# Kernel tuning notes

Hardware: AMD Instinct MI355X
Metric: run time of the kernel (lower is better)

Reference implementation:

```python
import jax, jax.numpy as jnp
import numpy as np

N = 50000          # nodes
E = 800000         # edges (avg degree 16)
T = 4              # edge types (edge_attr_dim)
H = 8              # heads
C1 = 16            # state_dim (per-head channels, layer 1)
C2 = 8             # out_dim  (per-head channels, layer 2)
D = 128            # node_attr_dim
NEG = -1e9         # masked-attention logit
LRELU_SLOPE = 0.2  # PyG GATConv default negative_slope


def setup_inputs() -> dict:
    key = jax.random.key(0)
    ks = jax.random.split(key, 12)
    x = jax.random.normal(ks[0], (N, D), jnp.float32)
    edge_src = jax.random.randint(ks[1], (E,), 0, N, jnp.int32)
    edge_dst = jax.random.randint(ks[2], (E,), 0, N, jnp.int32)
    edge_type = jax.random.randint(ks[3], (E,), 0, T, jnp.int32)
    W1 = jax.random.normal(ks[4], (T, D, H * C1), jnp.float32) * (1.0 / np.sqrt(D))
    a1_src = jax.random.normal(ks[5], (T, H, C1), jnp.float32) * 0.1
    a1_dst = jax.random.normal(ks[6], (T, H, C1), jnp.float32) * 0.1
    b1 = jnp.zeros((T, H * C1), jnp.float32)
    W2 = jax.random.normal(ks[7], (T, H * C1, H * C2), jnp.float32) * (1.0 / np.sqrt(H * C1))
    a2_src = jax.random.normal(ks[8], (T, H, C2), jnp.float32) * 0.1
    a2_dst = jax.random.normal(ks[9], (T, H, C2), jnp.float32) * 0.1
    b2 = jnp.zeros((T, H * C2), jnp.float32)
    return dict(x=x, edge_src=edge_src, edge_dst=edge_dst, edge_type=edge_type,
                W1=W1, a1_src=a1_src, a1_dst=a1_dst, b1=b1,
                W2=W2, a2_src=a2_src, a2_dst=a2_dst, b2=b2)


def gat_conv(x_in, W, a_src, a_dst, b, src, dst, mask, n):
    """One PyG-style GATConv (concat heads, eval mode) on masked edge list."""
    heads, c = a_src.shape
    h = (x_in @ W).reshape(n, heads, c)                       # [N,H,C]
    s_src = jnp.sum(h * a_src, axis=-1)                        # [N,H]
    s_dst = jnp.sum(h * a_dst, axis=-1)                        # [N,H]
    e = jax.nn.leaky_relu(s_src[src] + s_dst[dst], LRELU_SLOPE)  # [Et,H]
    e = jnp.where(mask[:, None], e, NEG)
    m = jax.ops.segment_max(e, dst, num_segments=n)            # [N,H]
    p = jnp.exp(e - m[dst]) * mask[:, None].astype(e.dtype)    # unnorm softmax
    denom = jax.ops.segment_sum(p, dst, num_segments=n)        # [N,H]
    msg = p[:, :, None] * h[src]                               # [Et,H,C]
    agg = jax.ops.segment_sum(msg, dst, num_segments=n)        # [N,H,C]
    out = agg / denom[:, :, None]
    return out.reshape(n, heads * c) + b


def reference(x, edge_src, edge_dst, edge_type, W1, a1_src, a1_dst, b1,
              W2, a2_src, a2_dst, b2):
    n = x.shape[0]
    loops = jnp.arange(n, dtype=edge_src.dtype)
    src = jnp.concatenate([edge_src, loops])   # self-loops appended (PyG default)
    dst = jnp.concatenate([edge_dst, loops])
    ones = jnp.ones((n,), bool)
    outs = []
    for t in range(T):
        mask = jnp.concatenate([edge_type == t, ones])
        h1 = gat_conv(x, W1[t], a1_src[t], a1_dst[t], b1[t], src, dst, mask, n)
        h1 = jax.nn.relu(h1)
        h2 = gat_conv(h1, W2[t], a2_src[t], a2_dst[t], b2[t], src, dst, mask, n)
        outs.append(h2)
    return jnp.concatenate(outs, axis=1)       # [N, T*H*C2]
```

## Files before the change

kernel.cpp:

```cpp
#include <hip/hip_runtime.h>
#include <cstddef>

constexpr int NN  = 50000;
constexpr int NE  = 800000;
constexpr int NT  = 4;
constexpr int NH  = 8;
constexpr int C1  = 16;
constexpr int C2  = 8;
constexpr int DD  = 128;
constexpr int HC1 = NH * C1;
constexpr int HC2 = NH * C2;
constexpr int NB  = NT * NN;
constexpr int CAP = 28;
constexpr float SLOPE = 0.2f;

constexpr int G_SCA1 = 1563;
constexpr int G_SCA2 = 1562;
constexpr int E_SPLIT = G_SCA1 * 256;
constexpr int G_CONV = NN * DD / 4 / 256;
constexpr int G_P1   = NT * 16384 / 256;
constexpr int G_P2   = NT * 8192 / 256;
constexpr int G_PREP = G_SCA1 + G_CONV + G_P1 + G_P2;
constexpr int G_GEMM = (NN + 63) / 64;
constexpr int G_GAT1 = NN / 16;
constexpr int G_GAT2 = (NN + 31) / 32;

using short8 = __attribute__((ext_vector_type(8))) short;
using f32x4  = __attribute__((ext_vector_type(4))) float;

__device__ __forceinline__ float lrelu(float x) { return x > 0.f ? x : SLOPE * x; }
__device__ __forceinline__ float bfl(unsigned u) { return __uint_as_float(u << 16); }
__device__ __forceinline__ float bfh(unsigned u) { return __uint_as_float(u & 0xffff0000u); }
__device__ __forceinline__ unsigned short f2bf(float f) {
    unsigned u = __float_as_uint(f);
    return (unsigned short)((u + 0x7fffu + ((u >> 16) & 1u)) >> 16);
}

__device__ __forceinline__ void scatter_edge(int i, const int* __restrict__ esrc,
        const int* __restrict__ edst, const int* __restrict__ etyp,
        unsigned* __restrict__ bkt) {
    int bk = etyp[i] * NN + edst[i];
    unsigned* bp = bkt + (size_t)bk * 16;
    int slot = atomicAdd(reinterpret_cast<int*>(bp), 1);
    if (slot < CAP)
        reinterpret_cast<unsigned short*>(bp)[2 + slot] = (unsigned short)esrc[i];
}

__global__ __launch_bounds__(256) void prep_kernel(const float* __restrict__ x,
        unsigned short* __restrict__ xb, const float* __restrict__ W1,
        unsigned short* __restrict__ wp1, const float* __restrict__ W2,
        unsigned short* __restrict__ wp2, const int* __restrict__ esrc,
        const int* __restrict__ edst, const int* __restrict__ etyp,
        unsigned* __restrict__ bkt) {
    const int b = blockIdx.x, tid = threadIdx.x;
    if (b < G_SCA1) {
        scatter_edge(b * 256 + tid, esrc, edst, etyp, bkt);
    } else if (b < G_SCA1 + G_CONV) {
        int i = (b - G_SCA1) * 256 + tid;
        float4 v = reinterpret_cast<const float4*>(x)[i];
        uint2 o;
        o.x = (unsigned)f2bf(v.x) | ((unsigned)f2bf(v.y) << 16);
        o.y = (unsigned)f2bf(v.z) | ((unsigned)f2bf(v.w) << 16);
        reinterpret_cast<uint2*>(xb)[i] = o;
    } else if (b < G_SCA1 + G_CONV + G_P1) {
        int i = (b - G_SCA1 - G_CONV) * 256 + tid;
        int t = i >> 14, r = i & 16383;
        int ntl = r >> 11, ks = (r >> 9) & 3, lane = (r >> 3) & 63, j = r & 7;
        int col = ntl * 16 + (lane & 15);
        int k   = ks * 32 + (lane >> 4) * 8 + j;
        wp1[i] = f2bf(W1[((size_t)t * DD + k) * HC1 + col]);
    } else {
        int i = (b - G_SCA1 - G_CONV - G_P1) * 256 + tid;
        int t = i >> 13, r = i & 8191;
        int ntl = r >> 11, ks = (r >> 9) & 3, lane = (r >> 3) & 63, j = r & 7;
        int col = ntl * 16 + (lane & 15);
        int k   = ks * 32 + (lane >> 4) * 8 + j;
        wp2[i] = f2bf(W2[((size_t)t * HC1 + k) * HC2 + col]);
    }
}

__device__ __forceinline__ void gemm1_body(int bx, int tid,
        const unsigned short* __restrict__ A, const unsigned short* __restrict__ Wp,
        const float* __restrict__ as, const float* __restrict__ ad,
        unsigned short* __restrict__ outb, float* __restrict__ ss,
        float* __restrict__ sd) {
    constexpr int J = HC1, CPH = C1, NTILE = J / 16;
    const int wave = tid >> 6;
    const int lane = tid & 63;
    const int q    = lane >> 4;
    const int c    = lane & 15;
    const int rowbase = bx * 64 + wave * 16;

    int arow = rowbase + c; if (arow >= NN) arow = NN - 1;
    const unsigned short* ap = A + (size_t)arow * DD + q * 8;
    short8 afrag[4];
    #pragma unroll
    for (int ks = 0; ks < 4; ++ks)
        afrag[ks] = *reinterpret_cast<const short8*>(ap + ks * 32);

    f32x4 acc[NTILE];
    #pragma unroll
    for (int ntl = 0; ntl < NTILE; ++ntl) acc[ntl] = (f32x4){0.f, 0.f, 0.f, 0.f};

    const short8* wp = reinterpret_cast<const short8*>(Wp) + lane;
    #pragma unroll
    for (int ntl = 0; ntl < NTILE; ++ntl)
        #pragma unroll
        for (int ks = 0; ks < 4; ++ks) {
            short8 b = wp[(ntl * 4 + ks) * 64];
            acc[ntl] = __builtin_amdgcn_mfma_f32_16x16x32_bf16(afrag[ks], b, acc[ntl], 0, 0, 0);
        }

    #pragma unroll
    for (int ntl = 0; ntl < NTILE; ++ntl) {
        int head = ntl;
        float av = as[head * CPH + c];
        float dv = ad[head * CPH + c];
        float t0[4], t1[4];
        #pragma unroll
        for (int reg = 0; reg < 4; ++reg) {
            int row = rowbase + q * 4 + reg;
            if (row < NN) outb[(size_t)row * J + ntl * 16 + c] = f2bf(acc[ntl][reg]);
            t0[reg] = acc[ntl][reg] * av;
            t1[reg] = acc[ntl][reg] * dv;
        }
        #pragma unroll
        for (int m = 1; m < CPH; m <<= 1)
            #pragma unroll
            for (int reg = 0; reg < 4; ++reg) {
                t0[reg] += __shfl_xor(t0[reg], m);
                t1[reg] += __shfl_xor(t1[reg], m);
            }
        if (c == 0) {
            #pragma unroll
            for (int reg = 0; reg < 4; ++reg) {
                int row = rowbase + q * 4 + reg;
                if (row < NN) { ss[row * NH + head] = t0[reg]; sd[row * NH + head] = t1[reg]; }
            }
        }
    }
}

__global__ __launch_bounds__(256) void scatgemm_kernel(
        const int* __restrict__ esrc, const int* __restrict__ edst,
        const int* __restrict__ etyp, unsigned* __restrict__ bkt,
        const unsigned short* __restrict__ xb, const unsigned short* __restrict__ wp1t,
        const float* __restrict__ as, const float* __restrict__ ad,
        unsigned short* __restrict__ h1, float* __restrict__ ss,
        float* __restrict__ sd) {
    const int b = blockIdx.x, tid = threadIdx.x;
    if (b < G_SCA2) {
        scatter_edge(E_SPLIT + b * 256 + tid, esrc, edst, etyp, bkt);
    } else {
        gemm1_body(b - G_SCA2, tid, xb, wp1t, as, ad, h1, ss, sd);
    }
}

template<int TPN>
__device__ __forceinline__ void gather_body(const unsigned* __restrict__ bkt, int bk,
        int q, int head, const float* __restrict__ ss, float sdn,
        const uint4* __restrict__ h4, float& den, float acc[8]) {
    const uint4* lp = reinterpret_cast<const uint4*>(bkt) + (size_t)bk * 4;
    uint4 w0 = lp[0], w1 = lp[1], w2 = lp[2], w3 = lp[3];
    int deg = (int)w0.x; if (deg > CAP) deg = CAP;
    unsigned ws[14] = {w0.y, w0.z, w0.w, w1.x, w1.y, w1.z, w1.w,
                       w2.x, w2.y, w2.z, w2.w, w3.x, w3.y, w3.z};
    #pragma unroll
    for (int c = 0; c < 7; ++c) {
        if (c * 4 >= deg) break;
        unsigned lo = ws[c * 2], hi = ws[c * 2 + 1];
        int sv[4] = {(int)(lo & 0xffff), (int)(lo >> 16),
                     (int)(hi & 0xffff), (int)(hi >> 16)};
        #pragma unroll
        for (int j = 0; j < 4; ++j) {
            if (c * 4 + j < deg) {
                int s = sv[j];
                float pp = __expf(lrelu(ss[s * NH + head] + sdn));
                uint4 hv = h4[(size_t)s * TPN + q];
                den += pp;
                acc[0] += pp * bfl(hv.x); acc[1] += pp * bfh(hv.x);
                acc[2] += pp * bfl(hv.y); acc[3] += pp * bfh(hv.y);
                acc[4] += pp * bfl(hv.z); acc[5] += pp * bfh(hv.z);
                acc[6] += pp * bfl(hv.w); acc[7] += pp * bfh(hv.w);
            }
        }
    }
}

__global__ __launch_bounds__(256) void g1g2_kernel(
        const unsigned* __restrict__ bkt, int t,
        const float* __restrict__ ss1, const float* __restrict__ sd1,
        const unsigned short* __restrict__ h1, const float* __restrict__ b1t,
        const unsigned short* __restrict__ wp2t,
        const float* __restrict__ as2, const float* __restrict__ ad2,
        unsigned short* __restrict__ h2, float* __restrict__ ss2,
        float* __restrict__ sd2) {
    __shared__ unsigned short lt[16][136];
    const int tid   = threadIdx.x;
    const int node0 = blockIdx.x * 16;
    const int nl    = tid >> 4;
    const int node  = node0 + nl;
    const int q     = tid & 15;
    const int head  = q >> 1;
    const int bk    = t * NN + node;
    const float sdn = sd1[node * NH + head];
    const uint4* __restrict__ h4 = reinterpret_cast<const uint4*>(h1);

    float p = __expf(lrelu(ss1[node * NH + head] + sdn));
    float den = p;
    uint4 hv = h4[(size_t)node * 16 + q];
    float acc[8];
    acc[0] = p * bfl(hv.x); acc[1] = p * bfh(hv.x);
    acc[2] = p * bfl(hv.y); acc[3] = p * bfh(hv.y);
    acc[4] = p * bfl(hv.z); acc[5] = p * bfh(hv.z);
    acc[6] = p * bfl(hv.w); acc[7] = p * bfh(hv.w);
    gather_body<16>(bkt, bk, q, head, ss1, sdn, h4, den, acc);

    float inv = 1.f / den;
    uint4 ov;
    {
        float o[8];
        #pragma unroll
        for (int i = 0; i < 8; ++i)
            o[i] = fmaxf(acc[i] * inv + b1t[q * 8 + i], 0.f);
        ov.x = (unsigned)f2bf(o[0]) | ((unsigned)f2bf(o[1]) << 16);
        ov.y = (unsigned)f2bf(o[2]) | ((unsigned)f2bf(o[3]) << 16);
        ov.z = (unsigned)f2bf(o[4]) | ((unsigned)f2bf(o[5]) << 16);
        ov.w = (unsigned)f2bf(o[6]) | ((unsigned)f2bf(o[7]) << 16);
    }
    *reinterpret_cast<uint4*>(&lt[nl][q * 8]) = ov;
    __syncthreads();

    const int wave = tid >> 6;
    const int lane = tid & 63;
    const int quad = lane >> 4;
    const int c    = lane & 15;
    short8 af[4];
    #pragma unroll
    for (int ks = 0; ks < 4; ++ks)
        af[ks] = *reinterpret_cast<const short8*>(&lt[c][ks * 32 + quad * 8]);
    f32x4 cacc = (f32x4){0.f, 0.f, 0.f, 0.f};
    const short8* wp = reinterpret_cast<const short8*>(wp2t) + lane;
    #pragma unroll
    for (int ks = 0; ks < 4; ++ks)
        cacc = __builtin_amdgcn_mfma_f32_16x16x32_bf16(af[ks], wp[(wave * 4 + ks) * 64], cacc, 0, 0, 0);

    const int col   = wave * 16 + c;
    const int head2 = col >> 3;
    const int cm    = c & 7;
    float av = as2[head2 * C2 + cm];
    float dv = ad2[head2 * C2 + cm];
    float t0[4], t1[4];
    #pragma unroll
    for (int reg = 0; reg < 4; ++reg) {
        int row = node0 + quad * 4 + reg;
        h2[(size_t)row * HC2 + col] = f2bf(cacc[reg]);
        t0[reg] = cacc[reg] * av;
        t1[reg] = cacc[reg] * dv;
    }
    #pragma unroll
    for (int m = 1; m < C2; m <<= 1)
        #pragma unroll
        for (int reg = 0; reg < 4; ++reg) {
            t0[reg] += __shfl_xor(t0[reg], m);
            t1[reg] += __shfl_xor(t1[reg], m);
        }
    if (cm == 0) {
        #pragma unroll
        for (int reg = 0; reg < 4; ++reg) {
            int row = node0 + quad * 4 + reg;
            ss2[row * NH + head2] = t0[reg];
            sd2[row * NH + head2] = t1[reg];
        }
    }
}

__global__ __launch_bounds__(256) void gat2gemm_kernel(
        const unsigned* __restrict__ bkt, int t,
        const float* __restrict__ ss2, const float* __restrict__ sd2,
        const unsigned short* __restrict__ h2, const float* __restrict__ b2t,
        float* __restrict__ out,
        const unsigned short* __restrict__ xb, const unsigned short* __restrict__ wp1n,
        const float* __restrict__ asn, const float* __restrict__ adn,
        unsigned short* __restrict__ h1, float* __restrict__ ss1,
        float* __restrict__ sd1) {
    const int b = blockIdx.x, tid = threadIdx.x;
    if (b >= G_GAT2) {
        gemm1_body(b - G_GAT2, tid, xb, wp1n, asn, adn, h1, ss1, sd1);
        return;
    }
    const int node = b * 32 + (tid >> 3);
    if (node >= NN) return;
    const int q    = tid & 7;
    const int head = q;
    const int bk   = t * NN + node;
    const float sdn = sd2[node * NH + head];
    const uint4* __restrict__ h4 = reinterpret_cast<const uint4*>(h2);

    float p = __expf(lrelu(ss2[node * NH + head] + sdn));
    float den = p;
    uint4 hv = h4[(size_t)node * 8 + q];
    float acc[8];
    acc[0] = p * bfl(hv.x); acc[1] = p * bfh(hv.x);
    acc[2] = p * bfl(hv.y); acc[3] = p * bfh(hv.y);
    acc[4] = p * bfl(hv.z); acc[5] = p * bfh(hv.z);
    acc[6] = p * bfl(hv.w); acc[7] = p * bfh(hv.w);
    gather_body<8>(bkt, bk, q, head, ss2, sdn, h4, den, acc);

    float inv = 1.f / den;
    float o[8];
    #pragma unroll
    for (int i = 0; i < 8; ++i) o[i] = acc[i] * inv + b2t[q * 8 + i];
    float* op = out + (size_t)node * (NT * HC2) + t * HC2 + q * 8;
    reinterpret_cast<float4*>(op)[0] = make_float4(o[0], o[1], o[2], o[3]);
    reinterpret_cast<float4*>(op)[1] = make_float4(o[4], o[5], o[6], o[7]);
}

extern "C" void kernel_launch(void* const* d_in, const int* in_sizes, int n_in,
                              void* d_out, int out_size, void* d_ws, size_t ws_size,
                              hipStream_t stream) {
    const float* x    = (const float*)d_in[0];
    const int*   esrc = (const int*)d_in[1];
    const int*   edst = (const int*)d_in[2];
    const int*   etyp = (const int*)d_in[3];
    const float* W1   = (const float*)d_in[4];
    const float* a1s  = (const float*)d_in[5];
    const float* a1d  = (const float*)d_in[6];
    const float* b1   = (const float*)d_in[7];
    const float* W2   = (const float*)d_in[8];
    const float* a2s  = (const float*)d_in[9];
    const float* a2d  = (const float*)d_in[10];
    const float* b2   = (const float*)d_in[11];
    float* out = (float*)d_out;

    char* base = (char*)d_ws;
    unsigned short* xb  = (unsigned short*)(base);
    unsigned short* h1b = (unsigned short*)(base + 12800000);
    unsigned short* h2b = (unsigned short*)(base + 25600000);
    float* ss1 = (float*)(base + 32000000);
    float* sd1 = (float*)(base + 33600000);
    float* ss2 = (float*)(base + 35200000);
    float* sd2 = (float*)(base + 36800000);
    unsigned* bkt = (unsigned*)(base + 38400000);
    unsigned short* wp1 = (unsigned short*)(base + 51200000);
    unsigned short* wp2 = (unsigned short*)(base + 51331072);

    dim3 blk(256);

    hipMemsetAsync(bkt, 0, (size_t)NB * 64, stream);
    hipLaunchKernelGGL(prep_kernel, dim3(G_PREP), blk, 0, stream,
                       x, xb, W1, wp1, W2, wp2, esrc, edst, etyp, bkt);
    hipLaunchKernelGGL(scatgemm_kernel, dim3(G_SCA2 + G_GEMM), blk, 0, stream,
                       esrc, edst, etyp, bkt,
                       xb, wp1, a1s, a1d, h1b, ss1, sd1);

    for (int t = 0; t < NT; ++t) {
        hipLaunchKernelGGL(g1g2_kernel, dim3(G_GAT1), blk, 0, stream,
                           bkt, t, ss1, sd1, h1b, b1 + t * HC1,
                           wp2 + (size_t)t * 8192,
                           a2s + t * NH * C2, a2d + t * NH * C2,
                           h2b, ss2, sd2);
        int tn = t + 1;
        int grid = G_GAT2 + (tn < NT ? G_GEMM : 0);
        hipLaunchKernelGGL(gat2gemm_kernel, dim3(grid), blk, 0, stream,
                           bkt, t, ss2, sd2, h2b, b2 + t * HC2, out,
                           xb, wp1 + (size_t)(tn < NT ? tn : 0) * 16384,
                           a1s + (tn < NT ? tn : 0) * NH * C1,
                           a1d + (tn < NT ? tn : 0) * NH * C1,
                           h1b, ss1, sd1);
    }
}
```

Baseline: 345.5 us.

## Pipeline GAT stages across edge types with double buffers and packed half scores

The per-type launch sequence becomes a five-step software pipeline. Each mega-kernel runs layer-1 gather+GEMM2 for type t, layer-2 gather for type t-1, and GEMM1 for type t+1, with h1/h2/score buffers double-buffered. The separate x-to-bf16 conversion pass is removed and the conversion happens inside GEMM1 loads. Attention scores are packed as half2 (src,dst), and buckets shrink to a 56-byte stride with capacity 26. The scatter handles four edges per thread. The main risks are lost precision in the half-stored scores and dropped edges at high degree from the smaller capacity.

```diff
diff --git a/kernel.cpp b/kernel.cpp
--- a/kernel.cpp
+++ b/kernel.cpp
@@ -1,4 +1,5 @@
 #include <hip/hip_runtime.h>
+#include <hip/hip_fp16.h>
 #include <cstddef>
 
 constexpr int NN  = 50000;
@@ -10,67 +11,68 @@
 constexpr int DD  = 128;
 constexpr int HC1 = NH * C1;
 constexpr int HC2 = NH * C2;
-constexpr int NB  = NT * NN;
-constexpr int CAP = 28;
+constexpr int CAP = 26;
+constexpr int BSTRIDE = 56;
 constexpr float SLOPE = 0.2f;
 
-constexpr int G_SCA1 = 1563;
-constexpr int G_SCA2 = 1562;
-constexpr int E_SPLIT = G_SCA1 * 256;
-constexpr int G_CONV = NN * DD / 4 / 256;
+constexpr int G_SCA  = 391;
+constexpr int E_SPLIT = G_SCA * 1024;
 constexpr int G_P1   = NT * 16384 / 256;
 constexpr int G_P2   = NT * 8192 / 256;
-constexpr int G_PREP = G_SCA1 + G_CONV + G_P1 + G_P2;
 constexpr int G_GEMM = (NN + 63) / 64;
 constexpr int G_GAT1 = NN / 16;
 constexpr int G_GAT2 = (NN + 31) / 32;
 
 using short8 = __attribute__((ext_vector_type(8))) short;
 using f32x4  = __attribute__((ext_vector_type(4))) float;
+typedef unsigned short u16;
 
 __device__ __forceinline__ float lrelu(float x) { return x > 0.f ? x : SLOPE * x; }
 __device__ __forceinline__ float bfl(unsigned u) { return __uint_as_float(u << 16); }
 __device__ __forceinline__ float bfh(unsigned u) { return __uint_as_float(u & 0xffff0000u); }
-__device__ __forceinline__ unsigned short f2bf(float f) {
+__device__ __forceinline__ u16 f2bf(float f) {
     unsigned u = __float_as_uint(f);
-    return (unsigned short)((u + 0x7fffu + ((u >> 16) & 1u)) >> 16);
-}
-
-__device__ __forceinline__ void scatter_edge(int i, const int* __restrict__ esrc,
+    return (u16)((u + 0x7fffu + ((u >> 16) & 1u)) >> 16);
+}
+
+__device__ __forceinline__ void scatter4(int e0, int elim, const int* __restrict__ esrc,
         const int* __restrict__ edst, const int* __restrict__ etyp,
         unsigned* __restrict__ bkt) {
-    int bk = etyp[i] * NN + edst[i];
-    unsigned* bp = bkt + (size_t)bk * 16;
-    int slot = atomicAdd(reinterpret_cast<int*>(bp), 1);
-    if (slot < CAP)
-        reinterpret_cast<unsigned short*>(bp)[2 + slot] = (unsigned short)esrc[i];
-}
-
-__global__ __launch_bounds__(256) void prep_kernel(const float* __restrict__ x,
-        unsigned short* __restrict__ xb, const float* __restrict__ W1,
-        unsigned short* __restrict__ wp1, const float* __restrict__ W2,
-        unsigned short* __restrict__ wp2, const int* __restrict__ esrc,
-        const int* __restrict__ edst, const int* __restrict__ etyp,
-        unsigned* __restrict__ bkt) {
+    int bk[4], src[4];
+    bool v[4];
+    #pragma unroll
+    for (int k = 0; k < 4; ++k) {
+        int i = e0 + k * 256;
+        v[k] = i < elim;
+        bk[k] = 0; src[k] = 0;
+        if (v[k]) { bk[k] = etyp[i] * NN + edst[i]; src[k] = esrc[i]; }
+    }
+    int slot[4];
+    #pragma unroll
+    for (int k = 0; k < 4; ++k)
+        if (v[k]) slot[k] = atomicAdd((int*)((char*)bkt + (size_t)bk[k] * BSTRIDE), 1);
+    #pragma unroll
+    for (int k = 0; k < 4; ++k)
+        if (v[k] && slot[k] < CAP)
+            ((u16*)((char*)bkt + (size_t)bk[k] * BSTRIDE))[2 + slot[k]] = (u16)src[k];
+}
+
+__global__ __launch_bounds__(256) void prep_kernel(const float* __restrict__ W1,
+        u16* __restrict__ wp1, const float* __restrict__ W2, u16* __restrict__ wp2,
+        const int* __restrict__ esrc, const int* __restrict__ edst,
+        const int* __restrict__ etyp, unsigned* __restrict__ bkt) {
     const int b = blockIdx.x, tid = threadIdx.x;
-    if (b < G_SCA1) {
-        scatter_edge(b * 256 + tid, esrc, edst, etyp, bkt);
-    } else if (b < G_SCA1 + G_CONV) {
-        int i = (b - G_SCA1) * 256 + tid;
-        float4 v = reinterpret_cast<const float4*>(x)[i];
-        uint2 o;
-        o.x = (unsigned)f2bf(v.x) | ((unsigned)f2bf(v.y) << 16);
-        o.y = (unsigned)f2bf(v.z) | ((unsigned)f2bf(v.w) << 16);
-        reinterpret_cast<uint2*>(xb)[i] = o;
-    } else if (b < G_SCA1 + G_CONV + G_P1) {
-        int i = (b - G_SCA1 - G_CONV) * 256 + tid;
+    if (b < G_SCA) {
+        scatter4(b * 1024 + tid, E_SPLIT, esrc, edst, etyp, bkt);
+    } else if (b < G_SCA + G_P1) {
+        int i = (b - G_SCA) * 256 + tid;
         int t = i >> 14, r = i & 16383;
         int ntl = r >> 11, ks = (r >> 9) & 3, lane = (r >> 3) & 63, j = r & 7;
         int col = ntl * 16 + (lane & 15);
         int k   = ks * 32 + (lane >> 4) * 8 + j;
         wp1[i] = f2bf(W1[((size_t)t * DD + k) * HC1 + col]);
     } else {
-        int i = (b - G_SCA1 - G_CONV - G_P1) * 256 + tid;
+        int i = (b - G_SCA - G_P1) * 256 + tid;
         int t = i >> 13, r = i & 8191;
         int ntl = r >> 11, ks = (r >> 9) & 3, lane = (r >> 3) & 63, j = r & 7;
         int col = ntl * 16 + (lane & 15);
@@ -79,12 +81,10 @@
     }
 }
 
-__device__ __forceinline__ void gemm1_body(int bx, int tid,
-        const unsigned short* __restrict__ A, const unsigned short* __restrict__ Wp,
-        const float* __restrict__ as, const float* __restrict__ ad,
-        unsigned short* __restrict__ outb, float* __restrict__ ss,
-        float* __restrict__ sd) {
-    constexpr int J = HC1, CPH = C1, NTILE = J / 16;
+__device__ __forceinline__ void gemm1_body(int bx, int tid, const float* __restrict__ x,
+        const u16* __restrict__ Wp, const float* __restrict__ as,
+        const float* __restrict__ ad, u16* __restrict__ h1w, __half2* __restrict__ s1w) {
+    constexpr int NTILE = HC1 / 16;
     const int wave = tid >> 6;
     const int lane = tid & 63;
     const int q    = lane >> 4;
@@ -92,16 +92,23 @@
     const int rowbase = bx * 64 + wave * 16;
 
     int arow = rowbase + c; if (arow >= NN) arow = NN - 1;
-    const unsigned short* ap = A + (size_t)arow * DD + q * 8;
+    const float* xp = x + (size_t)arow * DD + q * 8;
     short8 afrag[4];
     #pragma unroll
-    for (int ks = 0; ks < 4; ++ks)
-        afrag[ks] = *reinterpret_cast<const short8*>(ap + ks * 32);
+    for (int ks = 0; ks < 4; ++ks) {
+        float4 f0 = *reinterpret_cast<const float4*>(xp + ks * 32);
+        float4 f1 = *reinterpret_cast<const float4*>(xp + ks * 32 + 4);
+        short8 a;
+        a[0] = (short)f2bf(f0.x); a[1] = (short)f2bf(f0.y);
+        a[2] = (short)f2bf(f0.z); a[3] = (short)f2bf(f0.w);
+        a[4] = (short)f2bf(f1.x); a[5] = (short)f2bf(f1.y);
+        a[6] = (short)f2bf(f1.z); a[7] = (short)f2bf(f1.w);
+        afrag[ks] = a;
+    }
 
     f32x4 acc[NTILE];
     #pragma unroll
     for (int ntl = 0; ntl < NTILE; ++ntl) acc[ntl] = (f32x4){0.f, 0.f, 0.f, 0.f};
-
     const short8* wp = reinterpret_cast<const short8*>(Wp) + lane;
     #pragma unroll
     for (int ntl = 0; ntl < NTILE; ++ntl)
@@ -114,18 +121,18 @@
     #pragma unroll
     for (int ntl = 0; ntl < NTILE; ++ntl) {
         int head = ntl;
-        float av = as[head * CPH + c];
-        float dv = ad[head * CPH + c];
+        float av = as[head * C1 + c];
+        float dv = ad[head * C1 + c];
         float t0[4], t1[4];
         #pragma unroll
         for (int reg = 0; reg < 4; ++reg) {
             int row = rowbase + q * 4 + reg;
-            if (row < NN) outb[(size_t)row * J + ntl * 16 + c] = f2bf(acc[ntl][reg]);
+            if (row < NN) h1w[(size_t)row * HC1 + ntl * 16 + c] = f2bf(acc[ntl][reg]);
             t0[reg] = acc[ntl][reg] * av;
             t1[reg] = acc[ntl][reg] * dv;
         }
         #pragma unroll
-        for (int m = 1; m < CPH; m <<= 1)
+        for (int m = 1; m < C1; m <<= 1)
             #pragma unroll
             for (int reg = 0; reg < 4; ++reg) {
                 t0[reg] += __shfl_xor(t0[reg], m);
@@ -135,7 +142,9 @@
             #pragma unroll
             for (int reg = 0; reg < 4; ++reg) {
                 int row = rowbase + q * 4 + reg;
-                if (row < NN) { ss[row * NH + head] = t0[reg]; sd[row * NH + head] = t1[reg]; }
+                if (row < NN)
+                    s1w[row * NH + head] =
+                        __halves2half2(__float2half_rn(t0[reg]), __float2half_rn(t1[reg]));
             }
         }
     }
@@ -144,39 +153,39 @@
 __global__ __launch_bounds__(256) void scatgemm_kernel(
         const int* __restrict__ esrc, const int* __restrict__ edst,
         const int* __restrict__ etyp, unsigned* __restrict__ bkt,
-        const unsigned short* __restrict__ xb, const unsigned short* __restrict__ wp1t,
+        const float* __restrict__ x, const u16* __restrict__ wp1t,
         const float* __restrict__ as, const float* __restrict__ ad,
-        unsigned short* __restrict__ h1, float* __restrict__ ss,
-        float* __restrict__ sd) {
+        u16* __restrict__ h1, __half2* __restrict__ ss) {
     const int b = blockIdx.x, tid = threadIdx.x;
-    if (b < G_SCA2) {
-        scatter_edge(E_SPLIT + b * 256 + tid, esrc, edst, etyp, bkt);
+    if (b < G_SCA) {
+        scatter4(E_SPLIT + b * 1024 + tid, NE, esrc, edst, etyp, bkt);
     } else {
-        gemm1_body(b - G_SCA2, tid, xb, wp1t, as, ad, h1, ss, sd);
+        gemm1_body(b - G_SCA, tid, x, wp1t, as, ad, h1, ss);
     }
 }
 
 template<int TPN>
 __device__ __forceinline__ void gather_body(const unsigned* __restrict__ bkt, int bk,
-        int q, int head, const float* __restrict__ ss, float sdn,
+        int q, int head, const __half2* __restrict__ s, float sdn,
         const uint4* __restrict__ h4, float& den, float acc[8]) {
-    const uint4* lp = reinterpret_cast<const uint4*>(bkt) + (size_t)bk * 4;
-    uint4 w0 = lp[0], w1 = lp[1], w2 = lp[2], w3 = lp[3];
-    int deg = (int)w0.x; if (deg > CAP) deg = CAP;
-    unsigned ws[14] = {w0.y, w0.z, w0.w, w1.x, w1.y, w1.z, w1.w,
-                       w2.x, w2.y, w2.z, w2.w, w3.x, w3.y, w3.z};
+    const uint2* bp = reinterpret_cast<const uint2*>((const char*)bkt + (size_t)bk * BSTRIDE);
+    unsigned w[14];
+    #pragma unroll
+    for (int i = 0; i < 7; ++i) { uint2 u = bp[i]; w[2 * i] = u.x; w[2 * i + 1] = u.y; }
+    int deg = (int)w[0]; if (deg > CAP) deg = CAP;
     #pragma unroll
     for (int c = 0; c < 7; ++c) {
         if (c * 4 >= deg) break;
-        unsigned lo = ws[c * 2], hi = ws[c * 2 + 1];
+        unsigned lo = w[1 + 2 * c];
+        unsigned hi = (c < 6) ? w[2 + 2 * c] : 0u;
         int sv[4] = {(int)(lo & 0xffff), (int)(lo >> 16),
                      (int)(hi & 0xffff), (int)(hi >> 16)};
         #pragma unroll
         for (int j = 0; j < 4; ++j) {
             if (c * 4 + j < deg) {
-                int s = sv[j];
-                float pp = __expf(lrelu(ss[s * NH + head] + sdn));
-                uint4 hv = h4[(size_t)s * TPN + q];
+                int sn = sv[j];
+                float pp = __expf(lrelu(__low2float(s[sn * NH + head]) + sdn));
+                uint4 hv = h4[(size_t)sn * TPN + q];
                 den += pp;
                 acc[0] += pp * bfl(hv.x); acc[1] += pp * bfh(hv.x);
                 acc[2] += pp * bfl(hv.y); acc[3] += pp * bfh(hv.y);
@@ -187,26 +196,23 @@
     }
 }
 
-__global__ __launch_bounds__(256) void g1g2_kernel(
-        const unsigned* __restrict__ bkt, int t,
-        const float* __restrict__ ss1, const float* __restrict__ sd1,
-        const unsigned short* __restrict__ h1, const float* __restrict__ b1t,
-        const unsigned short* __restrict__ wp2t,
+__device__ __forceinline__ void g1g2_body(int bx, int tid, const unsigned* __restrict__ bkt,
+        int t, const __half2* __restrict__ s1r, const u16* __restrict__ h1r,
+        const float* __restrict__ b1t, const u16* __restrict__ wp2t,
         const float* __restrict__ as2, const float* __restrict__ ad2,
-        unsigned short* __restrict__ h2, float* __restrict__ ss2,
-        float* __restrict__ sd2) {
-    __shared__ unsigned short lt[16][136];
-    const int tid   = threadIdx.x;
-    const int node0 = blockIdx.x * 16;
+        u16* __restrict__ h2w, __half2* __restrict__ s2w) {
+    __shared__ u16 lt[16][136];
+    const int node0 = bx * 16;
     const int nl    = tid >> 4;
     const int node  = node0 + nl;
     const int q     = tid & 15;
     const int head  = q >> 1;
     const int bk    = t * NN + node;
-    const float sdn = sd1[node * NH + head];
-    const uint4* __restrict__ h4 = reinterpret_cast<const uint4*>(h1);
-
-    float p = __expf(lrelu(ss1[node * NH + head] + sdn));
+    const __half2 sown = s1r[node * NH + head];
+    const float sdn = __high2float(sown);
+    const uint4* __restrict__ h4 = reinterpret_cast<const uint4*>(h1r);
+
+    float p = __expf(lrelu(__low2float(sown) + sdn));
     float den = p;
     uint4 hv = h4[(size_t)node * 16 + q];
     float acc[8];
@@ -214,7 +220,7 @@
     acc[2] = p * bfl(hv.y); acc[3] = p * bfh(hv.y);
     acc[4] = p * bfl(hv.z); acc[5] = p * bfh(hv.z);
     acc[6] = p * bfl(hv.w); acc[7] = p * bfh(hv.w);
-    gather_body<16>(bkt, bk, q, head, ss1, sdn, h4, den, acc);
+    gather_body<16>(bkt, bk, q, head, s1r, sdn, h4, den, acc);
 
     float inv = 1.f / den;
     uint4 ov;
@@ -254,7 +260,7 @@
     #pragma unroll
     for (int reg = 0; reg < 4; ++reg) {
         int row = node0 + quad * 4 + reg;
-        h2[(size_t)row * HC2 + col] = f2bf(cacc[reg]);
+        h2w[(size_t)row * HC2 + col] = f2bf(cacc[reg]);
         t0[reg] = cacc[reg] * av;
         t1[reg] = cacc[reg] * dv;
     }
@@ -269,35 +275,25 @@
         #pragma unroll
         for (int reg = 0; reg < 4; ++reg) {
             int row = node0 + quad * 4 + reg;
-            ss2[row * NH + head2] = t0[reg];
-            sd2[row * NH + head2] = t1[reg];
-        }
-    }
-}
-
-__global__ __launch_bounds__(256) void gat2gemm_kernel(
-        const unsigned* __restrict__ bkt, int t,
-        const float* __restrict__ ss2, const float* __restrict__ sd2,
-        const unsigned short* __restrict__ h2, const float* __restrict__ b2t,
-        float* __restrict__ out,
-        const unsigned short* __restrict__ xb, const unsigned short* __restrict__ wp1n,
-        const float* __restrict__ asn, const float* __restrict__ adn,
-        unsigned short* __restrict__ h1, float* __restrict__ ss1,
-        float* __restrict__ sd1) {
-    const int b = blockIdx.x, tid = threadIdx.x;
-    if (b >= G_GAT2) {
-        gemm1_body(b - G_GAT2, tid, xb, wp1n, asn, adn, h1, ss1, sd1);
-        return;
-    }
-    const int node = b * 32 + (tid >> 3);
+            s2w[row * NH + head2] =
+                __halves2half2(__float2half_rn(t0[reg]), __float2half_rn(t1[reg]));
+        }
+    }
+}
+
+__device__ __forceinline__ void gat2_body(int bx, int tid, const unsigned* __restrict__ bkt,
+        int t, const __half2* __restrict__ s2r, const u16* __restrict__ h2r,
+        const float* __restrict__ b2t, float* __restrict__ out) {
+    const int node = bx * 32 + (tid >> 3);
     if (node >= NN) return;
     const int q    = tid & 7;
     const int head = q;
     const int bk   = t * NN + node;
-    const float sdn = sd2[node * NH + head];
-    const uint4* __restrict__ h4 = reinterpret_cast<const uint4*>(h2);
-
-    float p = __expf(lrelu(ss2[node * NH + head] + sdn));
+    const __half2 sown = s2r[node * NH + head];
+    const float sdn = __high2float(sown);
+    const uint4* __restrict__ h4 = reinterpret_cast<const uint4*>(h2r);
+
+    float p = __expf(lrelu(__low2float(sown) + sdn));
     float den = p;
     uint4 hv = h4[(size_t)node * 8 + q];
     float acc[8];
@@ -305,7 +301,7 @@
     acc[2] = p * bfl(hv.y); acc[3] = p * bfh(hv.y);
     acc[4] = p * bfl(hv.z); acc[5] = p * bfh(hv.z);
     acc[6] = p * bfl(hv.w); acc[7] = p * bfh(hv.w);
-    gather_body<8>(bkt, bk, q, head, ss2, sdn, h4, den, acc);
+    gather_body<8>(bkt, bk, q, head, s2r, sdn, h4, den, acc);
 
     float inv = 1.f / den;
     float o[8];
@@ -314,6 +310,27 @@
     float* op = out + (size_t)node * (NT * HC2) + t * HC2 + q * 8;
     reinterpret_cast<float4*>(op)[0] = make_float4(o[0], o[1], o[2], o[3]);
     reinterpret_cast<float4*>(op)[1] = make_float4(o[4], o[5], o[6], o[7]);
+}
+
+__global__ __launch_bounds__(256) void mega_kernel(
+        int ng1, int ngat2, const unsigned* __restrict__ bkt,
+        int t1, const __half2* __restrict__ s1r, const u16* __restrict__ h1r,
+        const float* __restrict__ b1t, const u16* __restrict__ wp2t,
+        const float* __restrict__ as2, const float* __restrict__ ad2,
+        u16* __restrict__ h2w, __half2* __restrict__ s2w,
+        int t2, const __half2* __restrict__ s2r, const u16* __restrict__ h2r,
+        const float* __restrict__ b2t, float* __restrict__ out,
+        const float* __restrict__ x, const u16* __restrict__ wp1n,
+        const float* __restrict__ as1, const float* __restrict__ ad1,
+        u16* __restrict__ h1w, __half2* __restrict__ s1w) {
+    const int b = blockIdx.x, tid = threadIdx.x;
+    if (b < ng1) {
+        g1g2_body(b, tid, bkt, t1, s1r, h1r, b1t, wp2t, as2, ad2, h2w, s2w);
+    } else if (b < ng1 + ngat2) {
+        gat2_body(b - ng1, tid, bkt, t2, s2r, h2r, b2t, out);
+    } else {
+        gemm1_body(b - ng1 - ngat2, tid, x, wp1n, as1, ad1, h1w, s1w);
+    }
 }
 
 extern "C" void kernel_launch(void* const* d_in, const int* in_sizes, int n_in,
@@ -334,39 +351,39 @@
     float* out = (float*)d_out;
 
     char* base = (char*)d_ws;
-    unsigned short* xb  = (unsigned short*)(base);
-    unsigned short* h1b = (unsigned short*)(base + 12800000);
-    unsigned short* h2b = (unsigned short*)(base + 25600000);
-    float* ss1 = (float*)(base + 32000000);
-    float* sd1 = (float*)(base + 33600000);
-    float* ss2 = (float*)(base + 35200000);
-    float* sd2 = (float*)(base + 36800000);
-    unsigned* bkt = (unsigned*)(base + 38400000);
-    unsigned short* wp1 = (unsigned short*)(base + 51200000);
-    unsigned short* wp2 = (unsigned short*)(base + 51331072);
+    u16*     h1d[2] = {(u16*)(base),            (u16*)(base + 12800000)};
+    u16*     h2d[2] = {(u16*)(base + 25600000), (u16*)(base + 32000000)};
+    __half2* s1d[2] = {(__half2*)(base + 38400000), (__half2*)(base + 40000000)};
+    __half2* s2d[2] = {(__half2*)(base + 41600000), (__half2*)(base + 43200000)};
+    unsigned* bkt = (unsigned*)(base + 44800000);
+    u16* wp1 = (u16*)(base + 56000000);
+    u16* wp2 = (u16*)(base + 56131072);
 
     dim3 blk(256);
 
-    hipMemsetAsync(bkt, 0, (size_t)NB * 64, stream);
-    hipLaunchKernelGGL(prep_kernel, dim3(G_PREP), blk, 0, stream,
-                       x, xb, W1, wp1, W2, wp2, esrc, edst, etyp, bkt);
-    hipLaunchKernelGGL(scatgemm_kernel, dim3(G_SCA2 + G_GEMM), blk, 0, stream,
+    hipMemsetAsync(bkt, 0, (size_t)200000 * BSTRIDE, stream);
+    hipLaunchKernelGGL(prep_kernel, dim3(G_SCA + G_P1 + G_P2), blk, 0, stream,
+                       W1, wp1, W2, wp2, esrc, edst, etyp, bkt);
+    hipLaunchKernelGGL(scatgemm_kernel, dim3(G_SCA + G_GEMM), blk, 0, stream,
                        esrc, edst, etyp, bkt,
-                       xb, wp1, a1s, a1d, h1b, ss1, sd1);
-
-    for (int t = 0; t < NT; ++t) {
-        hipLaunchKernelGGL(g1g2_kernel, dim3(G_GAT1), blk, 0, stream,
-                           bkt, t, ss1, sd1, h1b, b1 + t * HC1,
-                           wp2 + (size_t)t * 8192,
-                           a2s + t * NH * C2, a2d + t * NH * C2,
-                           h2b, ss2, sd2);
-        int tn = t + 1;
-        int grid = G_GAT2 + (tn < NT ? G_GEMM : 0);
-        hipLaunchKernelGGL(gat2gemm_kernel, dim3(grid), blk, 0, stream,
-                           bkt, t, ss2, sd2, h2b, b2 + t * HC2, out,
-                           xb, wp1 + (size_t)(tn < NT ? tn : 0) * 16384,
-                           a1s + (tn < NT ? tn : 0) * NH * C1,
-                           a1d + (tn < NT ? tn : 0) * NH * C1,
-                           h1b, ss1, sd1);
-    }
-}
+                       x, wp1, a1s, a1d, h1d[0], s1d[0]);
+
+    for (int t = 0; t < 5; ++t) {
+        int ng1   = (t < 4) ? G_GAT1 : 0;
+        int ngat2 = (t >= 1) ? G_GAT2 : 0;
+        int ngemm = (t < 3) ? G_GEMM : 0;
+        int tm = (t < 4) ? t : 3;
+        int tp = (t < 3) ? t + 1 : 0;
+        int t2 = (t >= 1) ? t - 1 : 0;
+        hipLaunchKernelGGL(mega_kernel, dim3(ng1 + ngat2 + ngemm), blk, 0, stream,
+                           ng1, ngat2, bkt,
+                           tm, s1d[tm & 1], h1d[tm & 1], b1 + tm * HC1,
+                           wp2 + (size_t)tm * 8192,
+                           a2s + tm * NH * C2, a2d + tm * NH * C2,
+                           h2d[tm & 1], s2d[tm & 1],
+                           t2, s2d[t2 & 1], h2d[t2 & 1], b2 + t2 * HC2, out,
+                           x, wp1 + (size_t)tp * 16384,
+                           a1s + tp * NH * C1, a1d + tp * NH * C1,
+                           h1d[tp & 1], s1d[tp & 1]);
+    }
+}
```

New measurement: 338.1 us. 1.02x faster.
